# Performance work log

Hardware: AMD Instinct MI355X
Metric: run time of the kernel (lower is better)

## Reference

```python
import jax, jax.numpy as jnp
import numpy as np

LEAK = 0.1
K = 16  # nsample

def leaky(x):
    return jnp.where(x > 0, x, LEAK * x)

def setup_inputs() -> dict:
    key = jax.random.key(0)
    ks = jax.random.split(key, 16)
    B, N, C, D = 2, 8192, 128, 128
    s = 0.05
    return {
        "xyz1": jax.random.normal(ks[0], (B, 3, N), jnp.float32),
        "xyz2": jax.random.normal(ks[1], (B, 3, N), jnp.float32),
        "points1": jax.random.normal(ks[2], (B, C, N), jnp.float32),
        "points2": jax.random.normal(ks[3], (B, C, N), jnp.float32),
        "W_t11": jax.random.normal(ks[4], (D, C), jnp.float32) * s,
        "b_t11": jax.random.normal(ks[5], (D,), jnp.float32) * s,
        "W_t22": jax.random.normal(ks[6], (D, C), jnp.float32) * s,
        "b_t22": jax.random.normal(ks[7], (D,), jnp.float32) * s,
        "W_pos": jax.random.normal(ks[8], (D, 3), jnp.float32) * s,
        "b_pos": jax.random.normal(ks[9], (D,), jnp.float32) * s,
        "W_mlp1": jax.random.normal(ks[10], (D, D), jnp.float32) * s,
        "b_mlp1": jax.random.normal(ks[11], (D,), jnp.float32) * s,
        "W_mlp2": jax.random.normal(ks[12], (D, D), jnp.float32) * s,
        "b_mlp2": jax.random.normal(ks[13], (D,), jnp.float32) * s,
    }

def reference(xyz1, xyz2, points1, points2,
              W_t11, b_t11, W_t22, b_t22, W_pos, b_pos,
              W_mlp1, b_mlp1, W_mlp2, b_mlp2):
    # xyz*: [B,3,N], points*: [B,C,N]
    x1 = jnp.transpose(xyz1, (0, 2, 1))  # [B,N1,3]
    x2 = jnp.transpose(xyz2, (0, 2, 1))  # [B,N2,3]
    # 1x1 conv1d (t11/t22) -> [B,N,D]
    p1 = jnp.einsum('dc,bcn->bnd', W_t11, points1) + b_t11
    p2 = jnp.einsum('dc,bcn->bnd', W_t22, points2) + b_t22
    # squared distances [B,N1,N2]
    dist = (jnp.sum(x1 ** 2, -1)[:, :, None]
            + jnp.sum(x2 ** 2, -1)[:, None, :]
            - 2.0 * jnp.einsum('bnc,bmc->bnm', x1, x2))
    _, idx = jax.lax.top_k(-dist, K)  # [B,N1,K] nearest neighbors
    gather = jax.vmap(lambda pts, ix: pts[ix])  # per-batch fancy index
    nbr_xyz = gather(x2, idx)   # [B,N1,K,3]
    g2 = gather(p2, idx)        # [B,N1,K,D]
    direction = nbr_xyz - x1[:, :, None, :]
    pos = jnp.einsum('dc,bnkc->bnkd', W_pos, direction) + b_pos
    new_pts = leaky(g2 + p1[:, :, None, :] + pos)  # BN is Identity (use_bn=False)
    new_pts = leaky(jnp.einsum('dc,bnkc->bnkd', W_mlp1, new_pts) + b_mlp1)
    new_pts = leaky(jnp.einsum('dc,bnkc->bnkd', W_mlp2, new_pts) + b_mlp2)
    out = jnp.max(new_pts, axis=2)  # max over nsample -> [B,N1,D]
    return jnp.transpose(out, (0, 2, 1))  # [B,D,N1] like torch
```

## Files before the change

### kernel.cpp

```cpp
#include <hip/hip_runtime.h>
#include <hip/hip_bf16.h>

static constexpr int B_ = 2;
static constexpr int N_ = 8192;
static constexpr int C_ = 128;
static constexpr int D_ = 128;
static constexpr int K_ = 16;

typedef float f32x4 __attribute__((ext_vector_type(4)));
typedef short s16x8 __attribute__((ext_vector_type(8)));

__device__ __forceinline__ float lrelu(float x) { return fmaxf(x, 0.1f * x); }
__device__ __forceinline__ unsigned short f2bf(float f) {
  __hip_bfloat16 h = __float2bfloat16(f);
  unsigned short u;
  __builtin_memcpy(&u, &h, 2);
  return u;
}
__device__ __forceinline__ float bfl(unsigned int u) { return __uint_as_float(u << 16); }
__device__ __forceinline__ float bfh(unsigned int u) { return __uint_as_float(u & 0xffff0000u); }
__device__ __forceinline__ float rfl(float v) {
  return __uint_as_float((unsigned int)__builtin_amdgcn_readfirstlane((int)__float_as_uint(v)));
}
__device__ __forceinline__ unsigned int mflip(unsigned int x) {
  return x ^ (((unsigned int)(((int)x) >> 31)) | 0x80000000u);
}

__global__ __launch_bounds__(256) void prep_kernel(
    const float* __restrict__ Wt11, const float* __restrict__ Wt22,
    const float* __restrict__ Wm1, const float* __restrict__ Wm2,
    const float* __restrict__ Wpos, const float* __restrict__ xyz2,
    const float* __restrict__ bt11, const float* __restrict__ bpos,
    float* __restrict__ Wt1T, float* __restrict__ Wt2T,
    unsigned short* __restrict__ w1bf, unsigned short* __restrict__ w2bf,
    float* __restrict__ wpx, float* __restrict__ wpy, float* __restrict__ wpz,
    float* __restrict__ b1c, f32x4* __restrict__ cand4) {
  int i = blockIdx.x * 256 + threadIdx.x;
  if (i < C_ * D_) {
    int d = i >> 7, c = i & 127;
    Wt1T[c * D_ + d] = Wt11[i];
    Wt2T[c * D_ + d] = Wt22[i];
    w1bf[i] = f2bf(Wm1[i]);
    w2bf[i] = f2bf(Wm2[i]);
    if (i < D_) {
      wpx[i] = Wpos[i * 3 + 0];
      wpy[i] = Wpos[i * 3 + 1];
      wpz[i] = Wpos[i * 3 + 2];
      b1c[i] = bt11[i] + bpos[i];
    }
    int bb = i >> 13, m = i & 8191;
    const float* s2 = xyz2 + (size_t)bb * 3 * N_;
    float x = s2[m], y = s2[N_ + m], z = s2[2 * N_ + m];
    f32x4 c4;
    c4[0] = -x; c4[1] = -y; c4[2] = -z;
    c4[3] = 0.5f * (x * x + y * y + z * z);
    cand4[(size_t)bb * N_ + m] = c4;
  }
}

__device__ __forceinline__ void conv_body(
    char* smem, int cbid,
    const float* __restrict__ pts, const float* __restrict__ WT,
    const float* __restrict__ bias, unsigned short* __restrict__ dst) {
  float (*tile)[32] = (float(*)[32])smem;
  int b = cbid >> 8;
  int n0 = (cbid & 255) << 5;
  int t = threadIdx.x;
  const float* src = pts + (size_t)b * C_ * N_ + n0;
  for (int i = t; i < C_ * 32; i += 256) {
    int c = i >> 5, nl = i & 31;
    tile[c][nl] = src[(size_t)c * N_ + nl];
  }
  __syncthreads();
  int w = t >> 6, lane = t & 63;
  int nl = lane & 31;
  int d0 = w * 32 + (lane >> 5) * 16;
  float acc[16];
#pragma unroll
  for (int j = 0; j < 16; ++j) acc[j] = 0.f;
  for (int c = 0; c < C_; ++c) {
    float x = tile[c][nl];
    const f32x4* wp = (const f32x4*)(WT + c * D_ + d0);
#pragma unroll
    for (int j = 0; j < 4; ++j) {
      f32x4 wv = wp[j];
#pragma unroll
      for (int q = 0; q < 4; ++q) acc[4 * j + q] += wv[q] * x;
    }
  }
  unsigned short* drow = dst + ((size_t)(b * N_ + n0 + nl)) * D_ + d0;
#pragma unroll
  for (int j8 = 0; j8 < 2; ++j8) {
    uint4 ov;
    unsigned int us[8];
#pragma unroll
    for (int e = 0; e < 8; ++e)
      us[e] = f2bf(acc[8 * j8 + e] + bias[d0 + 8 * j8 + e]);
    ov.x = us[0] | (us[1] << 16);
    ov.y = us[2] | (us[3] << 16);
    ov.z = us[4] | (us[5] << 16);
    ov.w = us[6] | (us[7] << 16);
    *(uint4*)(drow + 8 * j8) = ov;
  }
}

__device__ __forceinline__ void knn_body(
    char* smem, int kbid,
    const float* __restrict__ xyz1, const f32x4* __restrict__ cand4,
    int* __restrict__ idx_out) {
  float (*dmsh)[2][8][64] = (float(*)[2][8][64])smem;
  unsigned long long (*keybuf)[128] = (unsigned long long(*)[128])smem;
  unsigned int (*idxbuf)[8][128] = (unsigned int(*)[8][128])(smem + 8192);
  unsigned int (*icnt)[8] = (unsigned int(*)[8])(smem + 16384);

  int b = kbid >> 9;
  int q0 = (kbid & 511) << 4;
  int t = threadIdx.x;
  int w = t >> 6, lane = t & 63;
  int g = w >> 1, h = w & 1;
  int qbase = q0 + (g << 3);

  const float* s1 = xyz1 + (size_t)b * 3 * N_;
  const f32x4* cbf = cand4 + (size_t)b * N_;
  const f32x4* cb = cbf + (h << 12);

  if (t < 16) icnt[t >> 3][t & 7] = 0u;

  float qx[8], qy[8], qz[8], dmin[8];
#pragma unroll
  for (int qq = 0; qq < 8; ++qq) {
    int q = qbase + qq;
    qx[qq] = rfl(s1[q]);
    qy[qq] = rfl(s1[N_ + q]);
    qz[qq] = rfl(s1[2 * N_ + q]);
    dmin[qq] = 1e30f;
  }

  {
    f32x4 p0 = cb[lane], p1 = cb[64 + lane], p2 = cb[128 + lane], p3 = cb[192 + lane];
    auto proc1 = [&](f32x4 c) {
#pragma unroll
      for (int qq = 0; qq < 8; ++qq) {
        float s = __builtin_fmaf(c[0], qx[qq],
                  __builtin_fmaf(c[1], qy[qq],
                  __builtin_fmaf(c[2], qz[qq], c[3])));
        dmin[qq] = fminf(dmin[qq], s);
      }
    };
    for (int i = 0; i < 60; i += 4) {
      f32x4 c0 = p0; p0 = cb[((i + 4) << 6) + lane]; proc1(c0);
      f32x4 c1 = p1; p1 = cb[((i + 5) << 6) + lane]; proc1(c1);
      f32x4 c2 = p2; p2 = cb[((i + 6) << 6) + lane]; proc1(c2);
      f32x4 c3 = p3; p3 = cb[((i + 7) << 6) + lane]; proc1(c3);
    }
    proc1(p0); proc1(p1); proc1(p2); proc1(p3);
  }

#pragma unroll
  for (int qq = 0; qq < 8; ++qq) dmsh[g][h][qq][lane] = dmin[qq];
  __syncthreads();

  float thr[8];
#pragma unroll 1
  for (int qq = 0; qq < 8; ++qq) {
    unsigned int u0 = mflip(__float_as_uint(dmin[qq]));
    unsigned int u1 = mflip(__float_as_uint(dmsh[g][1 ^ h][qq][lane]));
    unsigned int sel = 0;
    for (int bit = 31; bit >= 0; --bit) {
      unsigned int trial = sel | (1u << bit);
      int c_lt = __popcll(__ballot(u0 < trial)) + __popcll(__ballot(u1 < trial));
      sel = (c_lt < 16) ? trial : sel;
    }
    unsigned int su = sel ^ ((sel & 0x80000000u) ? 0x80000000u : 0xFFFFFFFFu);
    float tf = __uint_as_float(su);
    thr[qq] = tf + (1e-4f + 4e-7f * fabsf(tf));
  }
  float thrmax = thr[0];
#pragma unroll
  for (int qq = 1; qq < 8; ++qq) thrmax = fmaxf(thrmax, thr[qq]);

  {
    f32x4 p0 = cb[lane], p1 = cb[64 + lane], p2 = cb[128 + lane], p3 = cb[192 + lane];
    int mo = (h << 12) + lane;
    auto proc2 = [&](f32x4 c, int m) {
      float s[8];
#pragma unroll
      for (int qq = 0; qq < 8; ++qq)
        s[qq] = __builtin_fmaf(c[0], qx[qq],
                __builtin_fmaf(c[1], qy[qq],
                __builtin_fmaf(c[2], qz[qq], c[3])));
      float mn = fminf(fminf(fminf(s[0], s[1]), fminf(s[2], s[3])),
                       fminf(fminf(s[4], s[5]), fminf(s[6], s[7])));
      if (__any(mn <= thrmax)) {
#pragma unroll
        for (int qq = 0; qq < 8; ++qq) {
          if (s[qq] <= thr[qq]) {
            unsigned int pos = atomicAdd(&icnt[g][qq], 1u);
            if (pos < 128u) idxbuf[g][qq][pos] = (unsigned int)m;
          }
        }
      }
    };
    for (int i = 0; i < 60; i += 4) {
      f32x4 c0 = p0; p0 = cb[((i + 4) << 6) + lane]; proc2(c0, mo + (i << 6));
      f32x4 c1 = p1; p1 = cb[((i + 5) << 6) + lane]; proc2(c1, mo + ((i + 1) << 6));
      f32x4 c2 = p2; p2 = cb[((i + 6) << 6) + lane]; proc2(c2, mo + ((i + 2) << 6));
      f32x4 c3 = p3; p3 = cb[((i + 7) << 6) + lane]; proc2(c3, mo + ((i + 3) << 6));
    }
    proc2(p0, mo + (60 << 6));
    proc2(p1, mo + (61 << 6));
    proc2(p2, mo + (62 << 6));
    proc2(p3, mo + (63 << 6));
  }
  __syncthreads();

#pragma unroll 1
  for (int j = 0; j < 4; ++j) {
    int wq = (w << 2) + j;
    int g2 = wq >> 3, qq2 = wq & 7;
    int q = q0 + wq;
    float qx2 = rfl(s1[q]);
    float qy2 = rfl(s1[N_ + q]);
    float qz2 = rfl(s1[2 * N_ + q]);
    int Cq = (int)icnt[g2][qq2];
    if (Cq > 128) Cq = 128;
    bool v0 = lane < Cq;
    unsigned int i0v = v0 ? idxbuf[g2][qq2][lane] : 0u;
    f32x4 c0 = cbf[i0v];
    float t0x = c0[0] + qx2, t0y = c0[1] + qy2, t0z = c0[2] + qz2;
    float d0 = __builtin_fmaf(t0x, t0x, __builtin_fmaf(t0y, t0y, t0z * t0z));
    unsigned long long key0 =
        v0 ? ((((unsigned long long)__float_as_uint(d0)) << 13) | i0v) : ~0ull;
    unsigned long long key1 = ~0ull;
    unsigned int i1v = 0;
    if (Cq > 64) {
      bool v1 = (lane + 64) < Cq;
      i1v = v1 ? idxbuf[g2][qq2][lane + 64] : 0u;
      f32x4 c1 = cbf[i1v];
      float t1x = c1[0] + qx2, t1y = c1[1] + qy2, t1z = c1[2] + qz2;
      float d1 = __builtin_fmaf(t1x, t1x, __builtin_fmaf(t1y, t1y, t1z * t1z));
      key1 = v1 ? ((((unsigned long long)__float_as_uint(d1)) << 13) | i1v) : ~0ull;
    }
    keybuf[w][lane] = key0;
    keybuf[w][lane + 64] = key1;
    int rank0 = 0, rank1 = 0;
    for (int j2 = 0; j2 < Cq; ++j2) {
      unsigned long long kj = keybuf[w][j2];
      rank0 += (kj < key0) ? 1 : 0;
      rank1 += (kj < key1) ? 1 : 0;
    }
    int* dst = idx_out + (((size_t)b * N_ + q) << 4);
    if (v0 && rank0 < K_) dst[rank0] = (int)i0v;
    if (key1 != ~0ull && rank1 < K_) dst[rank1] = (int)i1v;
  }
}

__global__ __launch_bounds__(256, 8) void fat_kernel(
    const float* __restrict__ xyz1, const f32x4* __restrict__ cand4,
    int* __restrict__ idx_out,
    const float* __restrict__ points1, const float* __restrict__ points2,
    const float* __restrict__ Wt1T, const float* __restrict__ Wt2T,
    const float* __restrict__ b1c, const float* __restrict__ bt22,
    unsigned short* __restrict__ p1b, unsigned short* __restrict__ p2b) {
  __shared__ __align__(16) char smem[16448];
  int bid = blockIdx.x;
  if (bid < 1024) {
    knn_body(smem, bid, xyz1, cand4, idx_out);
  } else if (bid < 1536) {
    conv_body(smem, bid - 1024, points1, Wt1T, b1c, p1b);
  } else {
    conv_body(smem, bid - 1536, points2, Wt2T, bt22, p2b);
  }
}

__global__ __launch_bounds__(256, 4) void fuse_kernel(
    const float* __restrict__ xyz1, const float* __restrict__ xyz2,
    const unsigned short* __restrict__ p1b, const unsigned short* __restrict__ p2b,
    const int* __restrict__ idxb,
    const unsigned short* __restrict__ w1bf, const unsigned short* __restrict__ w2bf,
    const float* __restrict__ wpx, const float* __restrict__ wpy,
    const float* __restrict__ wpz,
    const float* __restrict__ b1, const float* __restrict__ b2,
    float* __restrict__ out) {
  __shared__ unsigned char Abuf[32768];
  __shared__ float epib[4][8][32];

  int bid = blockIdx.x;
  int b = bid >> 10;
  int n0 = (bid & 1023) << 3;
  int t = threadIdx.x;
  int wv = t >> 6, lane = t & 63;
  int lrow = lane & 15, lk = lane >> 4;

  s16x8 wfr[2][4];
#pragma unroll
  for (int j2 = 0; j2 < 2; ++j2)
#pragma unroll
    for (int ks = 0; ks < 4; ++ks) {
      int row = wv * 32 + j2 * 16 + lrow;
      wfr[j2][ks] = *(const s16x8*)(w1bf + row * D_ + ks * 32 + lk * 8);
    }

  {
    int row = t >> 1, half = t & 1;
    int nl = row >> 4, kn = row & 15;
    int n = n0 + nl;
    int j = idxb[(((size_t)b * N_ + n) << 4) + kn];
    const float* s1 = xyz1 + (size_t)b * 3 * N_;
    const float* s2 = xyz2 + (size_t)b * 3 * N_;
    float dx = s2[j] - s1[n];
    float dy = s2[N_ + j] - s1[N_ + n];
    float dz = s2[2 * N_ + j] - s1[2 * N_ + n];
    const uint4* g2r = (const uint4*)(p2b + ((size_t)(b * N_ + j)) * D_ + half * 64);
    const uint4* p1r = (const uint4*)(p1b + ((size_t)(b * N_ + n)) * D_ + half * 64);
    int rswz = (row & 7) << 4;
#pragma unroll
    for (int it = 0; it < 8; ++it) {
      int dbase = half * 64 + it * 8;
      uint4 gv = g2r[it];
      uint4 pv = p1r[it];
      float g[8] = {bfl(gv.x), bfh(gv.x), bfl(gv.y), bfh(gv.y),
                    bfl(gv.z), bfh(gv.z), bfl(gv.w), bfh(gv.w)};
      float pp[8] = {bfl(pv.x), bfh(pv.x), bfl(pv.y), bfh(pv.y),
                     bfl(pv.z), bfh(pv.z), bfl(pv.w), bfh(pv.w)};
      f32x4 wxa = *(const f32x4*)(wpx + dbase);
      f32x4 wxb = *(const f32x4*)(wpx + dbase + 4);
      f32x4 wya = *(const f32x4*)(wpy + dbase);
      f32x4 wyb = *(const f32x4*)(wpy + dbase + 4);
      f32x4 wza = *(const f32x4*)(wpz + dbase);
      f32x4 wzb = *(const f32x4*)(wpz + dbase + 4);
      unsigned int us[8];
#pragma unroll
      for (int q = 0; q < 8; ++q) {
        float wx = q < 4 ? wxa[q] : wxb[q - 4];
        float wy = q < 4 ? wya[q] : wyb[q - 4];
        float wz = q < 4 ? wza[q] : wzb[q - 4];
        float v = __builtin_fmaf(wx, dx, __builtin_fmaf(wy, dy,
                  __builtin_fmaf(wz, dz, g[q] + pp[q])));
        us[q] = f2bf(lrelu(v));
      }
      uint4 val4;
      val4.x = us[0] | (us[1] << 16);
      val4.y = us[2] | (us[3] << 16);
      val4.z = us[4] | (us[5] << 16);
      val4.w = us[6] | (us[7] << 16);
      int off = (row << 8) + (dbase << 1);
      *(uint4*)(Abuf + (off ^ rswz)) = val4;
    }
  }
  __syncthreads();

  const f32x4 fzero = {0.f, 0.f, 0.f, 0.f};
  f32x4 acc[8][2];
#pragma unroll
  for (int m = 0; m < 8; ++m) { acc[m][0] = fzero; acc[m][1] = fzero; }

#pragma unroll
  for (int ks = 0; ks < 4; ++ks) {
#pragma unroll
    for (int m = 0; m < 8; ++m) {
      int rw = m * 16 + lrow;
      int off = (rw << 8) + (ks << 6) + (lk << 4);
      s16x8 afr = *(const s16x8*)(Abuf + (off ^ ((rw & 7) << 4)));
      acc[m][0] = __builtin_amdgcn_mfma_f32_16x16x32_bf16(afr, wfr[0][ks], acc[m][0], 0, 0, 0);
      acc[m][1] = __builtin_amdgcn_mfma_f32_16x16x32_bf16(afr, wfr[1][ks], acc[m][1], 0, 0, 0);
    }
  }
  __syncthreads();

#pragma unroll
  for (int j2 = 0; j2 < 2; ++j2)
#pragma unroll
    for (int ks = 0; ks < 4; ++ks) {
      int row = wv * 32 + j2 * 16 + lrow;
      wfr[j2][ks] = *(const s16x8*)(w2bf + row * D_ + ks * 32 + lk * 8);
    }

  {
    float bias1[2];
    bias1[0] = b1[wv * 32 + lrow];
    bias1[1] = b1[wv * 32 + 16 + lrow];
#pragma unroll
    for (int m = 0; m < 8; ++m)
#pragma unroll
      for (int j2 = 0; j2 < 2; ++j2)
#pragma unroll
        for (int r = 0; r < 4; ++r) {
          int rw = m * 16 + lk * 4 + r;
          int col = wv * 32 + j2 * 16 + lrow;
          unsigned short hv = f2bf(lrelu(acc[m][j2][r] + bias1[j2]));
          int off = (rw << 8) + (col << 1);
          *(unsigned short*)(Abuf + (off ^ ((rw & 7) << 4))) = hv;
        }
  }
  __syncthreads();

#pragma unroll
  for (int m = 0; m < 8; ++m) { acc[m][0] = fzero; acc[m][1] = fzero; }

#pragma unroll
  for (int ks = 0; ks < 4; ++ks) {
#pragma unroll
    for (int m = 0; m < 8; ++m) {
      int rw = m * 16 + lrow;
      int off = (rw << 8) + (ks << 6) + (lk << 4);
      s16x8 afr = *(const s16x8*)(Abuf + (off ^ ((rw & 7) << 4)));
      acc[m][0] = __builtin_amdgcn_mfma_f32_16x16x32_bf16(afr, wfr[0][ks], acc[m][0], 0, 0, 0);
      acc[m][1] = __builtin_amdgcn_mfma_f32_16x16x32_bf16(afr, wfr[1][ks], acc[m][1], 0, 0, 0);
    }
  }

  float bias2[2];
  bias2[0] = b2[wv * 32 + lrow];
  bias2[1] = b2[wv * 32 + 16 + lrow];
#pragma unroll
  for (int m = 0; m < 8; ++m) {
#pragma unroll
    for (int j2 = 0; j2 < 2; ++j2) {
      float mx = -1e30f;
#pragma unroll
      for (int r = 0; r < 4; ++r) mx = fmaxf(mx, lrelu(acc[m][j2][r] + bias2[j2]));
      mx = fmaxf(mx, __shfl_xor(mx, 16, 64));
      mx = fmaxf(mx, __shfl_xor(mx, 32, 64));
      if (lk == 0) epib[wv][m][j2 * 16 + lrow] = mx;
    }
  }
  {
    int dl = lane >> 1, nh = lane & 1;
    f32x4 o;
#pragma unroll
    for (int i2 = 0; i2 < 4; ++i2) o[i2] = epib[wv][nh * 4 + i2][dl];
    *(f32x4*)(out + ((size_t)(b * D_ + wv * 32 + dl)) * N_ + n0 + nh * 4) = o;
  }
}

extern "C" void kernel_launch(void* const* d_in, const int* in_sizes, int n_in,
                              void* d_out, int out_size, void* d_ws, size_t ws_size,
                              hipStream_t stream) {
  (void)in_sizes; (void)n_in; (void)out_size; (void)ws_size;
  const float* xyz1    = (const float*)d_in[0];
  const float* xyz2    = (const float*)d_in[1];
  const float* points1 = (const float*)d_in[2];
  const float* points2 = (const float*)d_in[3];
  const float* W_t11   = (const float*)d_in[4];
  const float* b_t11   = (const float*)d_in[5];
  const float* W_t22   = (const float*)d_in[6];
  const float* b_t22   = (const float*)d_in[7];
  const float* W_pos   = (const float*)d_in[8];
  const float* b_pos   = (const float*)d_in[9];
  const float* W_mlp1  = (const float*)d_in[10];
  const float* b_mlp1  = (const float*)d_in[11];
  const float* W_mlp2  = (const float*)d_in[12];
  const float* b_mlp2  = (const float*)d_in[13];
  float* out = (float*)d_out;

  char* ws = (char*)d_ws;
  unsigned short* p1b  = (unsigned short*)(ws);
  unsigned short* p2b  = (unsigned short*)(ws + 4194304);
  float* Wt1T          = (float*)(ws + 8388608);
  float* Wt2T          = (float*)(ws + 8454144);
  unsigned short* w1bf = (unsigned short*)(ws + 8519680);
  unsigned short* w2bf = (unsigned short*)(ws + 8552448);
  float* wpx           = (float*)(ws + 8585216);
  float* wpy           = (float*)(ws + 8585728);
  float* wpz           = (float*)(ws + 8586240);
  f32x4* cand4         = (f32x4*)(ws + 8586752);
  int* idxws           = (int*)(ws + 8848896);
  float* b1c           = (float*)(ws + 9897472);

  prep_kernel<<<64, 256, 0, stream>>>(W_t11, W_t22, W_mlp1, W_mlp2, W_pos, xyz2,
                                      b_t11, b_pos,
                                      Wt1T, Wt2T, w1bf, w2bf, wpx, wpy, wpz,
                                      b1c, cand4);
  fat_kernel<<<2048, 256, 0, stream>>>(xyz1, cand4, idxws,
                                       points1, points2, Wt1T, Wt2T,
                                       b1c, b_t22, p1b, p2b);
  fuse_kernel<<<B_ * 1024, 256, 0, stream>>>(xyz1, xyz2, p1b, p2b, idxws,
                                             w1bf, w2bf, wpx, wpy, wpz,
                                             b_mlp1, b_mlp2, out);
}
```

Measured before the change: 155.6 us.

## Split KNN candidate scan across four waves per block of eight queries

Each KNN block now handles 8 queries instead of 16, with all four waves splitting the 8192 candidates into quarters, rather than two wave pairs each covering half. The grid grows to 2048 KNN blocks, which gives more parallelism and shorter per-wave scan loops. The cost is that each candidate is loaded and distance-tested once per 8 queries instead of 16, doubling total candidate traffic. The threshold radix search also needs four ballots per bit instead of two.

```diff
diff --git a/kernel.cpp b/kernel.cpp
--- a/kernel.cpp
+++ b/kernel.cpp
@@ -108,28 +108,26 @@
     char* smem, int kbid,
     const float* __restrict__ xyz1, const f32x4* __restrict__ cand4,
     int* __restrict__ idx_out) {
-  float (*dmsh)[2][8][64] = (float(*)[2][8][64])smem;
+  float (*dmsh)[8][64] = (float(*)[8][64])smem;
   unsigned long long (*keybuf)[128] = (unsigned long long(*)[128])smem;
-  unsigned int (*idxbuf)[8][128] = (unsigned int(*)[8][128])(smem + 8192);
-  unsigned int (*icnt)[8] = (unsigned int(*)[8])(smem + 16384);
-
-  int b = kbid >> 9;
-  int q0 = (kbid & 511) << 4;
+  unsigned int (*idxbuf)[128] = (unsigned int(*)[128])(smem + 8192);
+  unsigned int* icnt = (unsigned int*)(smem + 12288);
+
+  int b = kbid >> 10;
+  int q0 = (kbid & 1023) << 3;
   int t = threadIdx.x;
   int w = t >> 6, lane = t & 63;
-  int g = w >> 1, h = w & 1;
-  int qbase = q0 + (g << 3);
 
   const float* s1 = xyz1 + (size_t)b * 3 * N_;
   const f32x4* cbf = cand4 + (size_t)b * N_;
-  const f32x4* cb = cbf + (h << 12);
-
-  if (t < 16) icnt[t >> 3][t & 7] = 0u;
+  const f32x4* cb = cbf + (w << 11);
+
+  if (t < 8) icnt[t] = 0u;
 
   float qx[8], qy[8], qz[8], dmin[8];
 #pragma unroll
   for (int qq = 0; qq < 8; ++qq) {
-    int q = qbase + qq;
+    int q = q0 + qq;
     qx[qq] = rfl(s1[q]);
     qy[qq] = rfl(s1[N_ + q]);
     qz[qq] = rfl(s1[2 * N_ + q]);
@@ -147,7 +145,7 @@
         dmin[qq] = fminf(dmin[qq], s);
       }
     };
-    for (int i = 0; i < 60; i += 4) {
+    for (int i = 0; i < 28; i += 4) {
       f32x4 c0 = p0; p0 = cb[((i + 4) << 6) + lane]; proc1(c0);
       f32x4 c1 = p1; p1 = cb[((i + 5) << 6) + lane]; proc1(c1);
       f32x4 c2 = p2; p2 = cb[((i + 6) << 6) + lane]; proc1(c2);
@@ -157,18 +155,21 @@
   }
 
 #pragma unroll
-  for (int qq = 0; qq < 8; ++qq) dmsh[g][h][qq][lane] = dmin[qq];
+  for (int qq = 0; qq < 8; ++qq) dmsh[w][qq][lane] = dmin[qq];
   __syncthreads();
 
   float thr[8];
 #pragma unroll 1
   for (int qq = 0; qq < 8; ++qq) {
-    unsigned int u0 = mflip(__float_as_uint(dmin[qq]));
-    unsigned int u1 = mflip(__float_as_uint(dmsh[g][1 ^ h][qq][lane]));
+    unsigned int u0 = mflip(__float_as_uint(dmsh[0][qq][lane]));
+    unsigned int u1 = mflip(__float_as_uint(dmsh[1][qq][lane]));
+    unsigned int u2 = mflip(__float_as_uint(dmsh[2][qq][lane]));
+    unsigned int u3 = mflip(__float_as_uint(dmsh[3][qq][lane]));
     unsigned int sel = 0;
     for (int bit = 31; bit >= 0; --bit) {
       unsigned int trial = sel | (1u << bit);
-      int c_lt = __popcll(__ballot(u0 < trial)) + __popcll(__ballot(u1 < trial));
+      int c_lt = __popcll(__ballot(u0 < trial)) + __popcll(__ballot(u1 < trial)) +
+                 __popcll(__ballot(u2 < trial)) + __popcll(__ballot(u3 < trial));
       sel = (c_lt < 16) ? trial : sel;
     }
     unsigned int su = sel ^ ((sel & 0x80000000u) ? 0x80000000u : 0xFFFFFFFFu);
@@ -181,7 +182,7 @@
 
   {
     f32x4 p0 = cb[lane], p1 = cb[64 + lane], p2 = cb[128 + lane], p3 = cb[192 + lane];
-    int mo = (h << 12) + lane;
+    int mo = (w << 11) + lane;
     auto proc2 = [&](f32x4 c, int m) {
       float s[8];
 #pragma unroll
@@ -195,37 +196,36 @@
 #pragma unroll
         for (int qq = 0; qq < 8; ++qq) {
           if (s[qq] <= thr[qq]) {
-            unsigned int pos = atomicAdd(&icnt[g][qq], 1u);
-            if (pos < 128u) idxbuf[g][qq][pos] = (unsigned int)m;
+            unsigned int pos = atomicAdd(&icnt[qq], 1u);
+            if (pos < 128u) idxbuf[qq][pos] = (unsigned int)m;
           }
         }
       }
     };
-    for (int i = 0; i < 60; i += 4) {
+    for (int i = 0; i < 28; i += 4) {
       f32x4 c0 = p0; p0 = cb[((i + 4) << 6) + lane]; proc2(c0, mo + (i << 6));
       f32x4 c1 = p1; p1 = cb[((i + 5) << 6) + lane]; proc2(c1, mo + ((i + 1) << 6));
       f32x4 c2 = p2; p2 = cb[((i + 6) << 6) + lane]; proc2(c2, mo + ((i + 2) << 6));
       f32x4 c3 = p3; p3 = cb[((i + 7) << 6) + lane]; proc2(c3, mo + ((i + 3) << 6));
     }
-    proc2(p0, mo + (60 << 6));
-    proc2(p1, mo + (61 << 6));
-    proc2(p2, mo + (62 << 6));
-    proc2(p3, mo + (63 << 6));
+    proc2(p0, mo + (28 << 6));
+    proc2(p1, mo + (29 << 6));
+    proc2(p2, mo + (30 << 6));
+    proc2(p3, mo + (31 << 6));
   }
   __syncthreads();
 
 #pragma unroll 1
-  for (int j = 0; j < 4; ++j) {
-    int wq = (w << 2) + j;
-    int g2 = wq >> 3, qq2 = wq & 7;
+  for (int j = 0; j < 2; ++j) {
+    int wq = (w << 1) + j;
     int q = q0 + wq;
     float qx2 = rfl(s1[q]);
     float qy2 = rfl(s1[N_ + q]);
     float qz2 = rfl(s1[2 * N_ + q]);
-    int Cq = (int)icnt[g2][qq2];
+    int Cq = (int)icnt[wq];
     if (Cq > 128) Cq = 128;
     bool v0 = lane < Cq;
-    unsigned int i0v = v0 ? idxbuf[g2][qq2][lane] : 0u;
+    unsigned int i0v = v0 ? idxbuf[wq][lane] : 0u;
     f32x4 c0 = cbf[i0v];
     float t0x = c0[0] + qx2, t0y = c0[1] + qy2, t0z = c0[2] + qz2;
     float d0 = __builtin_fmaf(t0x, t0x, __builtin_fmaf(t0y, t0y, t0z * t0z));
@@ -235,7 +235,7 @@
     unsigned int i1v = 0;
     if (Cq > 64) {
       bool v1 = (lane + 64) < Cq;
-      i1v = v1 ? idxbuf[g2][qq2][lane + 64] : 0u;
+      i1v = v1 ? idxbuf[wq][lane + 64] : 0u;
       f32x4 c1 = cbf[i1v];
       float t1x = c1[0] + qx2, t1y = c1[1] + qy2, t1z = c1[2] + qz2;
       float d1 = __builtin_fmaf(t1x, t1x, __builtin_fmaf(t1y, t1y, t1z * t1z));
@@ -262,14 +262,14 @@
     const float* __restrict__ Wt1T, const float* __restrict__ Wt2T,
     const float* __restrict__ b1c, const float* __restrict__ bt22,
     unsigned short* __restrict__ p1b, unsigned short* __restrict__ p2b) {
-  __shared__ __align__(16) char smem[16448];
+  __shared__ __align__(16) char smem[16384];
   int bid = blockIdx.x;
-  if (bid < 1024) {
+  if (bid < 2048) {
     knn_body(smem, bid, xyz1, cand4, idx_out);
-  } else if (bid < 1536) {
-    conv_body(smem, bid - 1024, points1, Wt1T, b1c, p1b);
+  } else if (bid < 2560) {
+    conv_body(smem, bid - 2048, points1, Wt1T, b1c, p1b);
   } else {
-    conv_body(smem, bid - 1536, points2, Wt2T, bt22, p2b);
+    conv_body(smem, bid - 2560, points2, Wt2T, bt22, p2b);
   }
 }
 
@@ -472,7 +472,7 @@
                                       b_t11, b_pos,
                                       Wt1T, Wt2T, w1bf, w2bf, wpx, wpy, wpz,
                                       b1c, cand4);
-  fat_kernel<<<2048, 256, 0, stream>>>(xyz1, cand4, idxws,
+  fat_kernel<<<3072, 256, 0, stream>>>(xyz1, cand4, idxws,
                                        points1, points2, Wt1T, Wt2T,
                                        b1c, b_t22, p1b, p2b);
   fuse_kernel<<<B_ * 1024, 256, 0, stream>>>(xyz1, xyz2, p1b, p2b, idxws,
```

New measurement: 178.7 us. 14.9% more time.
